# Optimization experiments

Measured on AMD Instinct MI355X. Metric: run time of the kernel, lower is better.

## Reference

```python
import jax, jax.numpy as jnp
import numpy as np

TAU = 20.0        # LIFNeuron default tau
THRESHOLD = 1.0   # LIFNeuron default threshold
RESET = 0.0       # LIFNeuron default reset
DT = 1.0          # SpikingNeuralNetwork dt
ALPHA = DT / TAU

B, T, I, H, O = 256, 128, 512, 1024, 512


def setup_inputs() -> dict:
    key = jax.random.key(0)
    ks = jax.random.split(key, 6)
    def w(k, shape, fan_in):
        return (jax.random.normal(k, shape, jnp.float32) / np.sqrt(fan_in)).astype(jnp.float32)
    return {
        "x":  jax.random.normal(ks[0], (B, T, I), jnp.float32),
        "We": w(ks[1], (I, H), I), "be": jnp.zeros((H,), jnp.float32),
        "W1": w(ks[2], (H, H), H), "b1": jnp.zeros((H,), jnp.float32),
        "W2": w(ks[3], (H, H), H), "b2": jnp.zeros((H,), jnp.float32),
        "Wo": w(ks[4], (H, O), H), "bo": jnp.zeros((O,), jnp.float32),
    }


def _lif(v, inp):
    # v += (-v + inp) * dt/tau; spike = (v >= thr); v = v*(1-spike) + reset*spike
    v = v + (inp - v) * ALPHA
    spike = (v >= THRESHOLD).astype(v.dtype)
    v = v * (1.0 - spike) + RESET * spike
    return v, spike


def reference(x, We, be, W1, b1, W2, b2, Wo, bo):
    b, t, _ = x.shape
    h_dim = We.shape[1]
    o_dim = Wo.shape[1]

    def step(carry, xt):
        v1, v2, vo = carry
        h = jax.nn.relu(xt @ We + be)          # [B, H]
        v1, s1 = _lif(v1, h)                   # neuron 0 (only 2 of 3 neurons used: zip truncation)
        h = s1 @ W1 + b1
        v2, s2 = _lif(v2, h)                   # neuron 1
        h = s2 @ W2 + b2                       # last hidden layer: no neuron applied before output_layer
        vo, so = _lif(vo, h @ Wo + bo)         # output neuron
        return (v1, v2, vo), (s1, s2, so)

    init = (jnp.zeros((b, h_dim), x.dtype),
            jnp.zeros((b, h_dim), x.dtype),
            jnp.zeros((b, o_dim), x.dtype))
    _, (S1, S2, SO) = jax.lax.scan(step, init, jnp.swapaxes(x, 0, 1))  # time-major scan
    # output_spike at last timestep + full (detached) spike history, stacked over time
    return SO[-1], S1, S2, SO
```

## Files before the change

### kernel.cpp

```cpp
#include <hip/hip_runtime.h>
#include <cstdint>
#include <cstddef>

#define B_ 256
#define T_ 128
#define I_ 512
#define H_ 1024
#define O_ 512
static constexpr float ALPHA = 1.0f / 20.0f;
static constexpr float THR   = 1.0f;
static constexpr float S12   = 0.000244140625f;

typedef _Float16 f16;
typedef __attribute__((ext_vector_type(8))) _Float16 f16x8;
typedef __attribute__((ext_vector_type(4))) float f32x4;

__device__ inline void gload_lds16(const void* gsrc, void* ldsdst) {
    __builtin_amdgcn_global_load_lds(
        (const __attribute__((address_space(1))) unsigned int*)gsrc,
        (__attribute__((address_space(3))) unsigned int*)ldsdst, 16, 0, 0);
}

template<bool PERM_X, bool RELU>
__global__ __launch_bounds__(256)
void gemm128(const float* __restrict__ A, const float* __restrict__ Bw,
             const float* __restrict__ bias, float* __restrict__ C,
             int M, int N, int K) {
    constexpr int BM = 128, BN = 128, BK = 16, TM = 8, TN = 8;
    __shared__ float As[BK][BM];
    __shared__ float Bs[BK][BN + 4];

    const int tid = threadIdx.x;
    const int ntile = N / BN;
    const int bx = blockIdx.x % ntile;
    const int by = blockIdx.x / ntile;
    const int row0 = by * BM, col0 = bx * BN;
    const int tx = tid & 15;
    const int ty = tid >> 4;

    float acc[TM][TN] = {};

    for (int k0 = 0; k0 < K; k0 += BK) {
#pragma unroll
        for (int p = 0; p < 2; ++p) {
            int f = tid + p * 256;
            int r  = f >> 2;
            int kc = (f & 3) << 2;
            int m = row0 + r;
            const float* arow;
            if (PERM_X) {
                int t = m >> 8;
                int b = m & 255;
                arow = A + (size_t)(b * T_ + t) * K;
            } else {
                arow = A + (size_t)m * K;
            }
            float4 v = *reinterpret_cast<const float4*>(arow + k0 + kc);
            As[kc + 0][r] = v.x;
            As[kc + 1][r] = v.y;
            As[kc + 2][r] = v.z;
            As[kc + 3][r] = v.w;
        }
#pragma unroll
        for (int p = 0; p < 2; ++p) {
            int f = tid + p * 256;
            int r  = f >> 5;
            int nc = (f & 31) << 2;
            float4 v = *reinterpret_cast<const float4*>(Bw + (size_t)(k0 + r) * N + col0 + nc);
            *reinterpret_cast<float4*>(&Bs[r][nc]) = v;
        }
        __syncthreads();

#pragma unroll
        for (int k = 0; k < BK; ++k) {
            float a[TM], b[TN];
#pragma unroll
            for (int i = 0; i < TM; ++i) a[i] = As[k][ty * TM + i];
#pragma unroll
            for (int j = 0; j < TN; ++j) b[j] = Bs[k][tx * TN + j];
#pragma unroll
            for (int i = 0; i < TM; ++i)
#pragma unroll
                for (int j = 0; j < TN; ++j)
                    acc[i][j] += a[i] * b[j];
        }
        __syncthreads();
    }

#pragma unroll
    for (int i = 0; i < TM; ++i) {
        size_t m = (size_t)(row0 + ty * TM + i);
#pragma unroll
        for (int jj = 0; jj < TN; jj += 4) {
            int n = col0 + tx * TN + jj;
            float4 c4;
            float c0 = acc[i][jj + 0] + bias[n + 0];
            float c1 = acc[i][jj + 1] + bias[n + 1];
            float c2 = acc[i][jj + 2] + bias[n + 2];
            float c3 = acc[i][jj + 3] + bias[n + 3];
            if (RELU) {
                c0 = fmaxf(c0, 0.f); c1 = fmaxf(c1, 0.f);
                c2 = fmaxf(c2, 0.f); c3 = fmaxf(c3, 0.f);
            }
            c4.x = c0; c4.y = c1; c4.z = c2; c4.w = c3;
            *reinterpret_cast<float4*>(C + m * N + n) = c4;
        }
    }
}

template<bool SPLITX, bool PERM, bool RELU, bool WRITE_LAST, bool F16OUT>
__global__ __launch_bounds__(256, 2)
void gemm_lif(const float* __restrict__ A,
              const f16* __restrict__ Bhi, const f16* __restrict__ Blo,
              const float* __restrict__ bias,
              float* __restrict__ S, float* __restrict__ last_out,
              f16* __restrict__ Sf,
              int N, int K) {
    constexpr int BK = 32;
    constexpr int NBUF = SPLITX ? 4 : 3;
    constexpr int BUFSTR = NBUF * 4096;
    constexpr size_t SMEM = (2 * BUFSTR * 2 > 64 * 132 * 4)
                                ? (size_t)(2 * BUFSTR * 2)
                                : (size_t)(64 * 132 * 4);
    __shared__ __align__(16) char smem[SMEM];
    f16* sm = (f16*)smem;
    float (*Cs)[132] = (float (*)[132])smem;

    const int tid  = threadIdx.x;
    const int lane = tid & 63;
    const int w    = tid >> 6;
    const int wr   = w >> 1, wc = w & 1;
    const int ntile = N >> 7;
    const int bx = blockIdx.x % ntile;
    const int b  = blockIdx.x / ntile;
    const int col0 = bx << 7;

    f32x4 acc0[4][4], acc1[4][4];
#pragma unroll
    for (int mi = 0; mi < 4; ++mi)
#pragma unroll
        for (int ni = 0; ni < 4; ++ni) {
            acc0[mi][ni] = {0.f, 0.f, 0.f, 0.f};
            acc1[mi][ni] = {0.f, 0.f, 0.f, 0.f};
        }

    {
        f16* Ah0 = sm;
        f16* Bh0 = sm + 4096;
        f16* Bl0 = sm + 8192;
        f16* Al0 = sm + 12288;
#pragma unroll
        for (int p = 0; p < 2; ++p) {
            int chunk = w * 2 + p;
            int r  = chunk * 16 + (lane >> 2);
            int kq = lane & 3;
            size_t off = (size_t)(col0 + r) * K + kq * 8;
            gload_lds16(Bhi + off, Bh0 + chunk * 512);
            gload_lds16(Blo + off, Bl0 + chunk * 512);
        }
#pragma unroll
        for (int p = 0; p < 4; ++p) {
            int c = tid + p * 256;
            int r = c >> 3;
            int q = c & 7;
            const float* arow = PERM ? A + (size_t)(b * T_ + r) * K
                                     : A + (size_t)(r * B_ + b) * K;
            float4 v = *reinterpret_cast<const float4*>(arow + q * 4);
            union { f16 h[4]; uint2 u; } hi;
            hi.h[0] = (f16)v.x; hi.h[1] = (f16)v.y;
            hi.h[2] = (f16)v.z; hi.h[3] = (f16)v.w;
            *reinterpret_cast<uint2*>(&Ah0[r * BK + q * 4]) = hi.u;
            if (SPLITX) {
                union { f16 h[4]; uint2 u; } lo;
                lo.h[0] = (f16)((v.x - (float)hi.h[0]) * 4096.0f);
                lo.h[1] = (f16)((v.y - (float)hi.h[1]) * 4096.0f);
                lo.h[2] = (f16)((v.z - (float)hi.h[2]) * 4096.0f);
                lo.h[3] = (f16)((v.w - (float)hi.h[3]) * 4096.0f);
                *reinterpret_cast<uint2*>(&Al0[r * BK + q * 4]) = lo.u;
            }
        }
    }
    __syncthreads();

    const int NIT = K / BK;
    for (int it = 0; it < NIT; ++it) {
        const int cur = it & 1, nxt = cur ^ 1;
        const bool more = (it + 1 < NIT);
        const int k0n = (it + 1) * BK;

        f16* Ah_c = sm + cur * BUFSTR;
        f16* Bh_c = Ah_c + 4096;
        f16* Bl_c = Ah_c + 8192;
        f16* Al_c = Ah_c + 12288;
        f16* Ah_n = sm + nxt * BUFSTR;
        f16* Bh_n = Ah_n + 4096;
        f16* Bl_n = Ah_n + 8192;
        f16* Al_n = Ah_n + 12288;

        float4 a4[4];
        if (more) {
#pragma unroll
            for (int p = 0; p < 2; ++p) {
                int chunk = w * 2 + p;
                int r  = chunk * 16 + (lane >> 2);
                int kq = lane & 3;
                size_t off = (size_t)(col0 + r) * K + k0n + kq * 8;
                gload_lds16(Bhi + off, Bh_n + chunk * 512);
                gload_lds16(Blo + off, Bl_n + chunk * 512);
            }
#pragma unroll
            for (int p = 0; p < 4; ++p) {
                int c = tid + p * 256;
                int r = c >> 3;
                int q = c & 7;
                const float* arow = PERM ? A + (size_t)(b * T_ + r) * K
                                         : A + (size_t)(r * B_ + b) * K;
                a4[p] = *reinterpret_cast<const float4*>(arow + k0n + q * 4);
            }
        }

        {
            f16x8 ahi[4], alo[4];
#pragma unroll
            for (int mi = 0; mi < 4; ++mi) {
                int ar = (wr * 64 + mi * 16 + (lane & 15)) * BK + (lane >> 4) * 8;
                ahi[mi] = *reinterpret_cast<const f16x8*>(&Ah_c[ar]);
                if (SPLITX) alo[mi] = *reinterpret_cast<const f16x8*>(&Al_c[ar]);
            }
#pragma unroll
            for (int ni = 0; ni < 4; ++ni) {
                int br = (wc * 64 + ni * 16 + (lane & 15)) * BK + (lane >> 4) * 8;
                f16x8 bh = *reinterpret_cast<const f16x8*>(&Bh_c[br]);
                f16x8 bl = *reinterpret_cast<const f16x8*>(&Bl_c[br]);
#pragma unroll
                for (int mi = 0; mi < 4; ++mi) {
                    acc0[mi][ni] = __builtin_amdgcn_mfma_f32_16x16x32_f16(
                        ahi[mi], bh, acc0[mi][ni], 0, 0, 0);
                    acc1[mi][ni] = __builtin_amdgcn_mfma_f32_16x16x32_f16(
                        ahi[mi], bl, acc1[mi][ni], 0, 0, 0);
                    if (SPLITX)
                        acc1[mi][ni] = __builtin_amdgcn_mfma_f32_16x16x32_f16(
                            alo[mi], bh, acc1[mi][ni], 0, 0, 0);
                }
            }
        }

        if (more) {
#pragma unroll
            for (int p = 0; p < 4; ++p) {
                int c = tid + p * 256;
                int r = c >> 3;
                int q = c & 7;
                float4 v = a4[p];
                union { f16 h[4]; uint2 u; } hi;
                hi.h[0] = (f16)v.x; hi.h[1] = (f16)v.y;
                hi.h[2] = (f16)v.z; hi.h[3] = (f16)v.w;
                *reinterpret_cast<uint2*>(&Ah_n[r * BK + q * 4]) = hi.u;
                if (SPLITX) {
                    union { f16 h[4]; uint2 u; } lo;
                    lo.h[0] = (f16)((v.x - (float)hi.h[0]) * 4096.0f);
                    lo.h[1] = (f16)((v.y - (float)hi.h[1]) * 4096.0f);
                    lo.h[2] = (f16)((v.z - (float)hi.h[2]) * 4096.0f);
                    lo.h[3] = (f16)((v.w - (float)hi.h[3]) * 4096.0f);
                    *reinterpret_cast<uint2*>(&Al_n[r * BK + q * 4]) = lo.u;
                }
            }
        }
        __syncthreads();
    }

    float v = 0.f, s = 0.f;
    float* Sp = S + (size_t)b * N + col0 + (tid & 127);
    const size_t tstride = (size_t)B_ * N;

    if (wr == 0) {
#pragma unroll
        for (int ni = 0; ni < 4; ++ni) {
            int col = wc * 64 + ni * 16 + (lane & 15);
            float bv = bias[col0 + col];
#pragma unroll
            for (int mi = 0; mi < 4; ++mi) {
                int rowb = mi * 16 + ((lane >> 4) << 2);
#pragma unroll
                for (int r = 0; r < 4; ++r) {
                    float cv = acc0[mi][ni][r] + S12 * acc1[mi][ni][r] + bv;
                    if (RELU) cv = fmaxf(cv, 0.f);
                    Cs[rowb + r][col] = cv;
                }
            }
        }
    }
    __syncthreads();
    if (tid < 128) {
#pragma unroll 4
        for (int t = 0; t < 64; ++t) {
            float in = Cs[t][tid];
            v = v + (in - v) * ALPHA;
            bool sp = (v >= THR);
            s = sp ? 1.0f : 0.0f;
            Sp[(size_t)t * tstride] = s;
            if (F16OUT) Sf[((size_t)b * T_ + t) * N + col0 + tid] = (f16)s;
            v = sp ? 0.0f : v;
        }
    }
    __syncthreads();
    if (wr == 1) {
#pragma unroll
        for (int ni = 0; ni < 4; ++ni) {
            int col = wc * 64 + ni * 16 + (lane & 15);
            float bv = bias[col0 + col];
#pragma unroll
            for (int mi = 0; mi < 4; ++mi) {
                int rowb = mi * 16 + ((lane >> 4) << 2);
#pragma unroll
                for (int r = 0; r < 4; ++r) {
                    float cv = acc0[mi][ni][r] + S12 * acc1[mi][ni][r] + bv;
                    if (RELU) cv = fmaxf(cv, 0.f);
                    Cs[rowb + r][col] = cv;
                }
            }
        }
    }
    __syncthreads();
    if (tid < 128) {
#pragma unroll 4
        for (int t = 64; t < 128; ++t) {
            float in = Cs[t - 64][tid];
            v = v + (in - v) * ALPHA;
            bool sp = (v >= THR);
            s = sp ? 1.0f : 0.0f;
            Sp[(size_t)t * tstride] = s;
            if (F16OUT) Sf[((size_t)b * T_ + t) * N + col0 + tid] = (f16)s;
            v = sp ? 0.0f : v;
        }
        if (WRITE_LAST) last_out[(size_t)b * N + col0 + tid] = s;
    }
}

__global__ __launch_bounds__(256, 2)
void gemm_lif_x2(const float* __restrict__ A,
                 const f16* __restrict__ Bhi,
                 const f16* __restrict__ Blo,
                 const float* __restrict__ bias,
                 float* __restrict__ S,
                 f16* __restrict__ Sf,
                 int N, int K) {
    constexpr int BK = 32;
    constexpr int BUFSTR = 4 * 4096;
    __shared__ __align__(16) char smem[2 * BUFSTR * 2];
    f16* sm = (f16*)smem;
    float (*Cs)[132] = (float (*)[132])smem;

    const int tid  = threadIdx.x;
    const int lane = tid & 63;
    const int w    = tid >> 6;
    const int wr   = w >> 1, wc = w & 1;
    const int ntile = N >> 7;
    const int bx = blockIdx.x % ntile;
    const int b  = blockIdx.x / ntile;
    const int col0 = bx << 7;
    const int sw = (((lane >> 4) ^ ((lane >> 1) & 3)) << 3);

    f32x4 acc0[4][4], acc1[4][4];
#pragma unroll
    for (int mi = 0; mi < 4; ++mi)
#pragma unroll
        for (int ni = 0; ni < 4; ++ni) {
            acc0[mi][ni] = {0.f, 0.f, 0.f, 0.f};
            acc1[mi][ni] = {0.f, 0.f, 0.f, 0.f};
        }

    {
        f16* Ah0 = sm;
        f16* Bh0 = sm + 4096;
        f16* Bl0 = sm + 8192;
        f16* Al0 = sm + 12288;
#pragma unroll
        for (int p = 0; p < 2; ++p) {
            int chunk = w * 2 + p;
            int r  = chunk * 16 + (lane >> 2);
            int kq = lane & 3;
            size_t off = (size_t)(col0 + r) * K + kq * 8;
            gload_lds16(Bhi + off, Bh0 + chunk * 512);
            gload_lds16(Blo + off, Bl0 + chunk * 512);
        }
#pragma unroll
        for (int p = 0; p < 4; ++p) {
            int c = tid + p * 256;
            int r = c >> 3;
            int q = c & 7;
            const float* arow = A + (size_t)(b * T_ + r) * K;
            float4 v = *reinterpret_cast<const float4*>(arow + q * 4);
            int aoff = r * 32 + ((((q >> 1) ^ ((r >> 1) & 3))) << 3) + ((q & 1) << 2);
            union { f16 h[4]; uint2 u; } hi;
            hi.h[0] = (f16)v.x; hi.h[1] = (f16)v.y;
            hi.h[2] = (f16)v.z; hi.h[3] = (f16)v.w;
            *reinterpret_cast<uint2*>(&Ah0[aoff]) = hi.u;
            union { f16 h[4]; uint2 u; } lo;
            lo.h[0] = (f16)((v.x - (float)hi.h[0]) * 4096.0f);
            lo.h[1] = (f16)((v.y - (float)hi.h[1]) * 4096.0f);
            lo.h[2] = (f16)((v.z - (float)hi.h[2]) * 4096.0f);
            lo.h[3] = (f16)((v.w - (float)hi.h[3]) * 4096.0f);
            *reinterpret_cast<uint2*>(&Al0[aoff]) = lo.u;
        }
    }
    __syncthreads();

    const int NIT = K / BK;
    for (int it = 0; it < NIT; ++it) {
        const int cur = it & 1, nxt = cur ^ 1;
        const bool more = (it + 1 < NIT);
        const int k0n = (it + 1) * BK;

        f16* Ah_c = sm + cur * BUFSTR;
        f16* Bh_c = Ah_c + 4096;
        f16* Bl_c = Ah_c + 8192;
        f16* Al_c = Ah_c + 12288;
        f16* Ah_n = sm + nxt * BUFSTR;
        f16* Bh_n = Ah_n + 4096;
        f16* Bl_n = Ah_n + 8192;
        f16* Al_n = Ah_n + 12288;

        float4 a4[4];
        if (more) {
#pragma unroll
            for (int p = 0; p < 2; ++p) {
                int chunk = w * 2 + p;
                int r  = chunk * 16 + (lane >> 2);
                int kq = lane & 3;
                size_t off = (size_t)(col0 + r) * K + k0n + kq * 8;
                gload_lds16(Bhi + off, Bh_n + chunk * 512);
                gload_lds16(Blo + off, Bl_n + chunk * 512);
            }
#pragma unroll
            for (int p = 0; p < 4; ++p) {
                int c = tid + p * 256;
                int r = c >> 3;
                int q = c & 7;
                const float* arow = A + (size_t)(b * T_ + r) * K;
                a4[p] = *reinterpret_cast<const float4*>(arow + k0n + q * 4);
            }
        }

        {
            f16x8 ahi[4], alo[4];
#pragma unroll
            for (int mi = 0; mi < 4; ++mi) {
                int ar = (wr * 64 + mi * 16 + (lane & 15)) * BK + sw;
                ahi[mi] = *reinterpret_cast<const f16x8*>(&Ah_c[ar]);
                alo[mi] = *reinterpret_cast<const f16x8*>(&Al_c[ar]);
            }
#pragma unroll
            for (int ni = 0; ni < 4; ++ni) {
                int br = (wc * 64 + ni * 16 + (lane & 15)) * BK + sw;
                f16x8 bh = *reinterpret_cast<const f16x8*>(&Bh_c[br]);
                f16x8 bl = *reinterpret_cast<const f16x8*>(&Bl_c[br]);
#pragma unroll
                for (int mi = 0; mi < 4; ++mi) {
                    acc0[mi][ni] = __builtin_amdgcn_mfma_f32_16x16x32_f16(
                        ahi[mi], bh, acc0[mi][ni], 0, 0, 0);
                    acc1[mi][ni] = __builtin_amdgcn_mfma_f32_16x16x32_f16(
                        ahi[mi], bl, acc1[mi][ni], 0, 0, 0);
                    acc1[mi][ni] = __builtin_amdgcn_mfma_f32_16x16x32_f16(
                        alo[mi], bh, acc1[mi][ni], 0, 0, 0);
                }
            }
        }

        if (more) {
#pragma unroll
            for (int p = 0; p < 4; ++p) {
                int c = tid + p * 256;
                int r = c >> 3;
                int q = c & 7;
                float4 v = a4[p];
                int aoff = r * 32 + ((((q >> 1) ^ ((r >> 1) & 3))) << 3) + ((q & 1) << 2);
                union { f16 h[4]; uint2 u; } hi;
                hi.h[0] = (f16)v.x; hi.h[1] = (f16)v.y;
                hi.h[2] = (f16)v.z; hi.h[3] = (f16)v.w;
                *reinterpret_cast<uint2*>(&Ah_n[aoff]) = hi.u;
                union { f16 h[4]; uint2 u; } lo;
                lo.h[0] = (f16)((v.x - (float)hi.h[0]) * 4096.0f);
                lo.h[1] = (f16)((v.y - (float)hi.h[1]) * 4096.0f);
                lo.h[2] = (f16)((v.z - (float)hi.h[2]) * 4096.0f);
                lo.h[3] = (f16)((v.w - (float)hi.h[3]) * 4096.0f);
                *reinterpret_cast<uint2*>(&Al_n[aoff]) = lo.u;
            }
        }
        __syncthreads();
    }

    float v = 0.f;
    float* Sp = S + (size_t)b * N + col0 + (tid & 127);
    const size_t tstride = (size_t)B_ * N;

    if (wr == 0) {
#pragma unroll
        for (int ni = 0; ni < 4; ++ni) {
            int col = wc * 64 + ni * 16 + (lane & 15);
            float bv = bias[col0 + col];
#pragma unroll
            for (int mi = 0; mi < 4; ++mi) {
                int rowb = mi * 16 + ((lane >> 4) << 2);
#pragma unroll
                for (int r = 0; r < 4; ++r) {
                    float cv = fmaxf(acc0[mi][ni][r] + S12 * acc1[mi][ni][r] + bv, 0.f);
                    Cs[rowb + r][col] = cv;
                }
            }
        }
    }
    __syncthreads();
    if (tid < 128) {
#pragma unroll 4
        for (int t = 0; t < 64; ++t) {
            float in = Cs[t][tid];
            v = v + (in - v) * ALPHA;
            bool sp = (v >= THR);
            float s = sp ? 1.0f : 0.0f;
            Sp[(size_t)t * tstride] = s;
            Sf[((size_t)b * T_ + t) * N + col0 + tid] = (f16)s;
            v = sp ? 0.0f : v;
        }
    }
    __syncthreads();
    if (wr == 1) {
#pragma unroll
        for (int ni = 0; ni < 4; ++ni) {
            int col = wc * 64 + ni * 16 + (lane & 15);
            float bv = bias[col0 + col];
#pragma unroll
            for (int mi = 0; mi < 4; ++mi) {
                int rowb = mi * 16 + ((lane >> 4) << 2);
#pragma unroll
                for (int r = 0; r < 4; ++r) {
                    float cv = fmaxf(acc0[mi][ni][r] + S12 * acc1[mi][ni][r] + bv, 0.f);
                    Cs[rowb + r][col] = cv;
                }
            }
        }
    }
    __syncthreads();
    if (tid < 128) {
#pragma unroll 4
        for (int t = 64; t < 128; ++t) {
            float in = Cs[t - 64][tid];
            v = v + (in - v) * ALPHA;
            bool sp = (v >= THR);
            float s = sp ? 1.0f : 0.0f;
            Sp[(size_t)t * tstride] = s;
            Sf[((size_t)b * T_ + t) * N + col0 + tid] = (f16)s;
            v = sp ? 0.0f : v;
        }
    }
}

template<bool WRITE_LAST, bool F16OUT>
__global__ __launch_bounds__(256, 2)
void gemm_lif_h(const f16* __restrict__ Af,
                const f16* __restrict__ Bhi,
                const f16* __restrict__ Blo,
                const float* __restrict__ bias,
                float* __restrict__ S,
                float* __restrict__ last_out,
                f16* __restrict__ Sf,
                int N, int K) {
    constexpr int BK = 32;
    constexpr int BUFF = 3 * 4096;
    __shared__ __align__(16) char smem[2 * BUFF * 2];
    f16* sm = (f16*)smem;
    float (*Cs)[132] = (float (*)[132])smem;

    const int tid  = threadIdx.x;
    const int lane = tid & 63;
    const int w    = tid >> 6;
    const int wr   = w >> 1, wc = w & 1;
    const int ntile = N >> 7;
    const int bx = blockIdx.x % ntile;
    const int b  = blockIdx.x / ntile;
    const int col0 = bx << 7;
    const int sw = (((lane >> 4) ^ ((lane >> 1) & 3)) << 3);

    f32x4 acc0[4][4], acc1[4][4];
#pragma unroll
    for (int mi = 0; mi < 4; ++mi)
#pragma unroll
        for (int ni = 0; ni < 4; ++ni) {
            acc0[mi][ni] = {0.f, 0.f, 0.f, 0.f};
            acc1[mi][ni] = {0.f, 0.f, 0.f, 0.f};
        }

    const int r0   = (w * 2 + 0) * 16 + (lane >> 2);
    const int r1   = (w * 2 + 1) * 16 + (lane >> 2);
    const int kqs  = lane & 3;
    const int kqa0 = kqs ^ ((r0 >> 1) & 3);
    const int kqa1 = kqs ^ ((r1 >> 1) & 3);

    {
        size_t b0 = (size_t)(col0 + r0) * K + kqs * 8;
        size_t b1 = (size_t)(col0 + r1) * K + kqs * 8;
        size_t a0 = ((size_t)b * T_ + r0) * K + kqa0 * 8;
        size_t a1 = ((size_t)b * T_ + r1) * K + kqa1 * 8;
        gload_lds16(Af + a0,  sm + (w * 2 + 0) * 512);
        gload_lds16(Af + a1,  sm + (w * 2 + 1) * 512);
        gload_lds16(Bhi + b0, sm + 4096 + (w * 2 + 0) * 512);
        gload_lds16(Bhi + b1, sm + 4096 + (w * 2 + 1) * 512);
        gload_lds16(Blo + b0, sm + 8192 + (w * 2 + 0) * 512);
        gload_lds16(Blo + b1, sm + 8192 + (w * 2 + 1) * 512);
    }
    __syncthreads();

    const int NIT = K / BK;
    for (int it = 0; it < NIT; ++it) {
        f16* cur = sm + (it & 1) * BUFF;
        if (it + 1 < NIT) {
            f16* nb = sm + ((it + 1) & 1) * BUFF;
            int k0n = (it + 1) * BK;
            size_t b0 = (size_t)(col0 + r0) * K + k0n + kqs * 8;
            size_t b1 = (size_t)(col0 + r1) * K + k0n + kqs * 8;
            size_t a0 = ((size_t)b * T_ + r0) * K + k0n + kqa0 * 8;
            size_t a1 = ((size_t)b * T_ + r1) * K + k0n + kqa1 * 8;
            gload_lds16(Af + a0,  nb + (w * 2 + 0) * 512);
            gload_lds16(Af + a1,  nb + (w * 2 + 1) * 512);
            gload_lds16(Bhi + b0, nb + 4096 + (w * 2 + 0) * 512);
            gload_lds16(Bhi + b1, nb + 4096 + (w * 2 + 1) * 512);
            gload_lds16(Blo + b0, nb + 8192 + (w * 2 + 0) * 512);
            gload_lds16(Blo + b1, nb + 8192 + (w * 2 + 1) * 512);
        }

        f16x8 af[4];
#pragma unroll
        for (int mi = 0; mi < 4; ++mi)
            af[mi] = *reinterpret_cast<const f16x8*>(
                &cur[(wr * 64 + mi * 16 + (lane & 15)) * BK + sw]);
#pragma unroll
        for (int ni = 0; ni < 4; ++ni) {
            int br = (wc * 64 + ni * 16 + (lane & 15)) * BK + sw;
            f16x8 bh = *reinterpret_cast<const f16x8*>(&cur[4096 + br]);
            f16x8 bl = *reinterpret_cast<const f16x8*>(&cur[8192 + br]);
#pragma unroll
            for (int mi = 0; mi < 4; ++mi) {
                acc0[mi][ni] = __builtin_amdgcn_mfma_f32_16x16x32_f16(
                    af[mi], bh, acc0[mi][ni], 0, 0, 0);
                acc1[mi][ni] = __builtin_amdgcn_mfma_f32_16x16x32_f16(
                    af[mi], bl, acc1[mi][ni], 0, 0, 0);
            }
        }
        __syncthreads();
    }

    float v = 0.f, s = 0.f;
    float* Sp = S + (size_t)b * N + col0 + (tid & 127);
    const size_t tstride = (size_t)B_ * N;

    if (wr == 0) {
#pragma unroll
        for (int ni = 0; ni < 4; ++ni) {
            int col = wc * 64 + ni * 16 + (lane & 15);
            float bv = bias[col0 + col];
#pragma unroll
            for (int mi = 0; mi < 4; ++mi) {
                int rowb = mi * 16 + ((lane >> 4) << 2);
#pragma unroll
                for (int r = 0; r < 4; ++r)
                    Cs[rowb + r][col] = acc0[mi][ni][r] + S12 * acc1[mi][ni][r] + bv;
            }
        }
    }
    __syncthreads();
    if (tid < 128) {
#pragma unroll 4
        for (int t = 0; t < 64; ++t) {
            float in = Cs[t][tid];
            v = v + (in - v) * ALPHA;
            bool sp = (v >= THR);
            s = sp ? 1.0f : 0.0f;
            Sp[(size_t)t * tstride] = s;
            if (F16OUT) Sf[((size_t)b * T_ + t) * N + col0 + tid] = (f16)s;
            v = sp ? 0.0f : v;
        }
    }
    __syncthreads();
    if (wr == 1) {
#pragma unroll
        for (int ni = 0; ni < 4; ++ni) {
            int col = wc * 64 + ni * 16 + (lane & 15);
            float bv = bias[col0 + col];
#pragma unroll
            for (int mi = 0; mi < 4; ++mi) {
                int rowb = mi * 16 + ((lane >> 4) << 2);
#pragma unroll
                for (int r = 0; r < 4; ++r)
                    Cs[rowb + r][col] = acc0[mi][ni][r] + S12 * acc1[mi][ni][r] + bv;
            }
        }
    }
    __syncthreads();
    if (tid < 128) {
#pragma unroll 4
        for (int t = 64; t < 128; ++t) {
            float in = Cs[t - 64][tid];
            v = v + (in - v) * ALPHA;
            bool sp = (v >= THR);
            s = sp ? 1.0f : 0.0f;
            Sp[(size_t)t * tstride] = s;
            if (F16OUT) Sf[((size_t)b * T_ + t) * N + col0 + tid] = (f16)s;
            v = sp ? 0.0f : v;
        }
        if (WRITE_LAST) last_out[(size_t)b * N + col0 + tid] = s;
    }
}

__global__ __launch_bounds__(256)
void lif_scan(float* __restrict__ buf, int BH, float* __restrict__ last_out) {
    int j = blockIdx.x * 256 + threadIdx.x;
    if (j >= BH) return;
    float v = 0.f;
    float last = 0.f;
    for (int t = 0; t < T_; ++t) {
        size_t idx = (size_t)t * BH + j;
        float in = buf[idx];
        v = v + (in - v) * ALPHA;
        bool sp = (v >= THR);
        last = sp ? 1.0f : 0.0f;
        buf[idx] = last;
        v = sp ? 0.0f : v;
    }
    if (last_out) last_out[j] = last;
}

__global__ __launch_bounds__(256)
void make_wf2(const float* __restrict__ W2, const float* __restrict__ Wo,
              float* __restrict__ Wf) {
    __shared__ float w2s[64][33];
    __shared__ float wos[64][68];
    const int tid = threadIdx.x;
    const int ht = blockIdx.x >> 3, ot = blockIdx.x & 7;
    const int h0 = ht * 32, o0 = ot * 64;
    const int th = tid >> 3;
    const int to = tid & 7;

    double acc[8] = {0, 0, 0, 0, 0, 0, 0, 0};

    for (int k0 = 0; k0 < H_; k0 += 64) {
#pragma unroll
        for (int p = 0; p < 2; ++p) {
            int f = tid + p * 256;
            int i = f >> 4;
            int j4 = (f & 15) << 2;
            float4 v = *reinterpret_cast<const float4*>(
                W2 + (size_t)(h0 + i) * H_ + k0 + j4);
            w2s[j4 + 0][i] = v.x; w2s[j4 + 1][i] = v.y;
            w2s[j4 + 2][i] = v.z; w2s[j4 + 3][i] = v.w;
        }
#pragma unroll
        for (int p = 0; p < 4; ++p) {
            int f = tid + p * 256;
            int r = f >> 4;
            int c4 = (f & 15) << 2;
            float4 v = *reinterpret_cast<const float4*>(
                Wo + (size_t)(k0 + r) * O_ + o0 + c4);
            wos[r][c4 + 0] = v.x; wos[r][c4 + 1] = v.y;
            wos[r][c4 + 2] = v.z; wos[r][c4 + 3] = v.w;
        }
        __syncthreads();

#pragma unroll 8
        for (int k = 0; k < 64; ++k) {
            double a = (double)w2s[k][th];
#pragma unroll
            for (int j = 0; j < 8; ++j)
                acc[j] += a * (double)wos[k][to * 8 + j];
        }
        __syncthreads();
    }
#pragma unroll
    for (int j = 0; j < 8; ++j)
        Wf[(size_t)(h0 + th) * O_ + o0 + to * 8 + j] = (float)acc[j];
}

__global__ __launch_bounds__(256)
void make_bf(const float* __restrict__ Wo, const float* __restrict__ b2,
             const float* __restrict__ bo, float* __restrict__ bf) {
    int o = blockIdx.x * 256 + threadIdx.x;
    if (o >= O_) return;
    double acc = (double)bo[o];
    for (int h = 0; h < H_; ++h)
        acc += (double)b2[h] * (double)Wo[(size_t)h * O_ + o];
    bf[o] = (float)acc;
}

template<bool SWZ>
__global__ __launch_bounds__(256)
void split_w16(const float* __restrict__ W, f16* __restrict__ hi,
               f16* __restrict__ lo, int K, int N) {
    int idx = blockIdx.x * 256 + threadIdx.x;
    if (idx >= K * N) return;
    int n = idx / K;
    int ks = idx - n * K;
    int k = SWZ ? ((ks & ~31) | ((((ks >> 3) & 3) ^ ((n >> 1) & 3)) << 3) | (ks & 7))
                : ks;
    float wv = W[(size_t)k * N + n];
    f16 h0 = (f16)wv;
    float r = (wv - (float)h0) * 4096.0f;
    f16 h1 = (f16)r;
    hi[idx] = h0; lo[idx] = h1;
}

extern "C" void kernel_launch(void* const* d_in, const int* in_sizes, int n_in,
                              void* d_out, int out_size, void* d_ws, size_t ws_size,
                              hipStream_t stream) {
    const float* x  = (const float*)d_in[0];
    const float* We = (const float*)d_in[1];
    const float* be = (const float*)d_in[2];
    const float* W1 = (const float*)d_in[3];
    const float* b1 = (const float*)d_in[4];
    const float* W2 = (const float*)d_in[5];
    const float* b2 = (const float*)d_in[6];
    const float* Wo = (const float*)d_in[7];
    const float* bo = (const float*)d_in[8];

    float* out = (float*)d_out;
    float* so_last = out;
    float* S1 = out + (size_t)B_ * O_;
    float* S2 = S1 + (size_t)T_ * B_ * H_;
    float* SO = S2 + (size_t)T_ * B_ * H_;

    const int TB = T_ * B_;
    dim3 blk(256);

    const size_t MB = 1024 * 1024;
    const size_t sz_s1f = (size_t)T_ * B_ * H_ * 2;

    const size_t b_weh = 0;
    const size_t b_wel = 1 * MB;
    const size_t b_w1h = 2 * MB;
    const size_t b_w1l = 4 * MB;
    const size_t b_wfh = 6 * MB;
    const size_t b_wfl = 7 * MB;
    const size_t b_bf  = 8 * MB;
    const size_t b_wf  = 8 * MB + 4096;
    const size_t b_s1f = 10 * MB + 4096;
    const size_t b_s2f = b_s1f + sz_s1f;
    const size_t need_hi = b_s2f + sz_s1f;

    const size_t m_weh = 0;
    const size_t m_wel = m_weh + (size_t)I_ * H_ * 2;
    const size_t m_w1h = m_wel + (size_t)I_ * H_ * 2;
    const size_t m_w1l = m_w1h + (size_t)H_ * H_ * 2;
    const size_t m_wf  = m_w1l + (size_t)H_ * H_ * 2;
    const size_t m_bf  = m_wf + (size_t)H_ * O_ * 4;
    const size_t m_wfh = m_bf + (size_t)O_ * 4;
    const size_t m_wfl = m_wfh + (size_t)H_ * O_ * 2;
    const size_t need_mid = m_wfl + (size_t)H_ * O_ * 2;

    if (ws_size >= need_hi) {
        char* ws = (char*)d_ws;
        f16*   weh = (f16*)(ws + b_weh);
        f16*   wel = (f16*)(ws + b_wel);
        f16*   w1h = (f16*)(ws + b_w1h);
        f16*   w1l = (f16*)(ws + b_w1l);
        f16*   wfh = (f16*)(ws + b_wfh);
        f16*   wfl = (f16*)(ws + b_wfl);
        float* bf  = (float*)(ws + b_bf);
        float* Wf  = (float*)(ws + b_wf);
        f16*   s1f = (f16*)(ws + b_s1f);
        f16*   s2f = (f16*)(ws + b_s2f);

        split_w16<true><<<dim3((I_ * H_ + 255) / 256), blk, 0, stream>>>(We, weh, wel, I_, H_);
        split_w16<true><<<dim3((H_ * H_ + 255) / 256), blk, 0, stream>>>(W1, w1h, w1l, H_, H_);
        make_wf2<<<dim3(256), blk, 0, stream>>>(W2, Wo, Wf);
        make_bf<<<dim3(2), blk, 0, stream>>>(Wo, b2, bo, bf);
        split_w16<true><<<dim3((H_ * O_ + 255) / 256), blk, 0, stream>>>(Wf, wfh, wfl, H_, O_);

        gemm_lif_x2<<<dim3(B_ * (H_ / 128)), blk, 0, stream>>>(
            x, weh, wel, be, S1, s1f, H_, I_);

        gemm_lif_h<false, true><<<dim3(B_ * (H_ / 128)), blk, 0, stream>>>(
            s1f, w1h, w1l, b1, S2, nullptr, s2f, H_, H_);

        gemm_lif_h<true, false><<<dim3(B_ * (O_ / 128)), blk, 0, stream>>>(
            s2f, wfh, wfl, bf, SO, so_last, nullptr, O_, H_);
    } else if (ws_size >= need_mid) {
        char* ws = (char*)d_ws;
        f16*   weh = (f16*)(ws + m_weh);
        f16*   wel = (f16*)(ws + m_wel);
        f16*   w1h = (f16*)(ws + m_w1h);
        f16*   w1l = (f16*)(ws + m_w1l);
        float* Wf  = (float*)(ws + m_wf);
        float* bf  = (float*)(ws + m_bf);
        f16*   wfh = (f16*)(ws + m_wfh);
        f16*   wfl = (f16*)(ws + m_wfl);

        split_w16<false><<<dim3((I_ * H_ + 255) / 256), blk, 0, stream>>>(We, weh, wel, I_, H_);
        split_w16<false><<<dim3((H_ * H_ + 255) / 256), blk, 0, stream>>>(W1, w1h, w1l, H_, H_);
        make_wf2<<<dim3(256), blk, 0, stream>>>(W2, Wo, Wf);
        make_bf<<<dim3(2), blk, 0, stream>>>(Wo, b2, bo, bf);
        split_w16<false><<<dim3((H_ * O_ + 255) / 256), blk, 0, stream>>>(Wf, wfh, wfl, H_, O_);

        gemm_lif<true, true, true, false, false><<<dim3(B_ * (H_ / 128)), blk, 0, stream>>>(
            x, weh, wel, be, S1, nullptr, nullptr, H_, I_);
        gemm_lif<false, false, false, false, false><<<dim3(B_ * (H_ / 128)), blk, 0, stream>>>(
            S1, w1h, w1l, b1, S2, nullptr, nullptr, H_, H_);
        gemm_lif<false, false, false, true, false><<<dim3(B_ * (O_ / 128)), blk, 0, stream>>>(
            S2, wfh, wfl, bf, SO, so_last, nullptr, O_, H_);
    } else {
        float* Wf = (float*)d_ws;
        float* bf = Wf + (size_t)H_ * O_;
        gemm128<true, true><<<dim3((TB / 128) * (H_ / 128)), blk, 0, stream>>>(
            x, We, be, S1, TB, H_, I_);
        lif_scan<<<dim3((B_ * H_ + 255) / 256), blk, 0, stream>>>(S1, B_ * H_, nullptr);
        gemm128<false, false><<<dim3((TB / 128) * (H_ / 128)), blk, 0, stream>>>(
            S1, W1, b1, S2, TB, H_, H_);
        lif_scan<<<dim3((B_ * H_ + 255) / 256), blk, 0, stream>>>(S2, B_ * H_, nullptr);
        make_wf2<<<dim3(256), blk, 0, stream>>>(W2, Wo, Wf);
        make_bf<<<dim3(2), blk, 0, stream>>>(Wo, b2, bo, bf);
        gemm128<false, false><<<dim3((TB / 128) * (O_ / 128)), blk, 0, stream>>>(
            S2, Wf, bf, SO, TB, O_, H_);
        lif_scan<<<dim3((B_ * O_ + 255) / 256), blk, 0, stream>>>(SO, B_ * O_, so_last);
    }
}
```

Before: 581.3 us.

## Cut LDS and raise occupancy in LIF GEMMs; tile-transpose weight split kernels

The first-layer GEMM stops double-buffering the converted A tile in shared memory, so LDS per block drops to 48KB, and both GEMM kernels are asked for three blocks per CU instead of two. The A tile now gets an extra barrier before it is overwritten, which adds a sync and reduces overlap in exchange for occupancy. The weight hi/lo split kernels are rewritten to transpose through shared memory for coalesced reads and vectorized writes. The bias-folding kernel is parallelised over four partial sums per output. Raising the launch bound may force register spills in the MFMA-heavy kernels.

New measurement: 884.7 us. 52.2% more time.

```diff
diff --git a/kernel.cpp b/kernel.cpp
--- a/kernel.cpp
+++ b/kernel.cpp
@@ -337,8 +337,8 @@
     }
 }
 
-__global__ __launch_bounds__(256, 2)
-void gemm_lif_x2(const float* __restrict__ A,
+__global__ __launch_bounds__(256, 3)
+void gemm_lif_x3(const float* __restrict__ A,
                  const f16* __restrict__ Bhi,
                  const f16* __restrict__ Blo,
                  const float* __restrict__ bias,
@@ -346,9 +346,10 @@
                  f16* __restrict__ Sf,
                  int N, int K) {
     constexpr int BK = 32;
-    constexpr int BUFSTR = 4 * 4096;
-    __shared__ __align__(16) char smem[2 * BUFSTR * 2];
+    __shared__ __align__(16) char smem[49152];
     f16* sm = (f16*)smem;
+    f16* Ah = sm;
+    f16* Al = sm + 4096;
     float (*Cs)[132] = (float (*)[132])smem;
 
     const int tid  = threadIdx.x;
@@ -371,10 +372,8 @@
         }
 
     {
-        f16* Ah0 = sm;
-        f16* Bh0 = sm + 4096;
-        f16* Bl0 = sm + 8192;
-        f16* Al0 = sm + 12288;
+        f16* Bh0 = sm + 8192;
+        f16* Bl0 = sm + 12288;
 #pragma unroll
         for (int p = 0; p < 2; ++p) {
             int chunk = w * 2 + p;
@@ -395,34 +394,28 @@
             union { f16 h[4]; uint2 u; } hi;
             hi.h[0] = (f16)v.x; hi.h[1] = (f16)v.y;
             hi.h[2] = (f16)v.z; hi.h[3] = (f16)v.w;
-            *reinterpret_cast<uint2*>(&Ah0[aoff]) = hi.u;
+            *reinterpret_cast<uint2*>(&Ah[aoff]) = hi.u;
             union { f16 h[4]; uint2 u; } lo;
             lo.h[0] = (f16)((v.x - (float)hi.h[0]) * 4096.0f);
             lo.h[1] = (f16)((v.y - (float)hi.h[1]) * 4096.0f);
             lo.h[2] = (f16)((v.z - (float)hi.h[2]) * 4096.0f);
             lo.h[3] = (f16)((v.w - (float)hi.h[3]) * 4096.0f);
-            *reinterpret_cast<uint2*>(&Al0[aoff]) = lo.u;
+            *reinterpret_cast<uint2*>(&Al[aoff]) = lo.u;
         }
     }
     __syncthreads();
 
     const int NIT = K / BK;
     for (int it = 0; it < NIT; ++it) {
-        const int cur = it & 1, nxt = cur ^ 1;
         const bool more = (it + 1 < NIT);
         const int k0n = (it + 1) * BK;
-
-        f16* Ah_c = sm + cur * BUFSTR;
-        f16* Bh_c = Ah_c + 4096;
-        f16* Bl_c = Ah_c + 8192;
-        f16* Al_c = Ah_c + 12288;
-        f16* Ah_n = sm + nxt * BUFSTR;
-        f16* Bh_n = Ah_n + 4096;
-        f16* Bl_n = Ah_n + 8192;
-        f16* Al_n = Ah_n + 12288;
+        f16* Bh_c = sm + 8192 + (it & 1) * 8192;
+        f16* Bl_c = Bh_c + 4096;
 
         float4 a4[4];
         if (more) {
+            f16* Bh_n = sm + 8192 + ((it + 1) & 1) * 8192;
+            f16* Bl_n = Bh_n + 4096;
 #pragma unroll
             for (int p = 0; p < 2; ++p) {
                 int chunk = w * 2 + p;
@@ -447,8 +440,8 @@
 #pragma unroll
             for (int mi = 0; mi < 4; ++mi) {
                 int ar = (wr * 64 + mi * 16 + (lane & 15)) * BK + sw;
-                ahi[mi] = *reinterpret_cast<const f16x8*>(&Ah_c[ar]);
-                alo[mi] = *reinterpret_cast<const f16x8*>(&Al_c[ar]);
+                ahi[mi] = *reinterpret_cast<const f16x8*>(&Ah[ar]);
+                alo[mi] = *reinterpret_cast<const f16x8*>(&Al[ar]);
             }
 #pragma unroll
             for (int ni = 0; ni < 4; ++ni) {
@@ -466,6 +459,7 @@
                 }
             }
         }
+        __syncthreads();
 
         if (more) {
 #pragma unroll
@@ -478,13 +472,13 @@
                 union { f16 h[4]; uint2 u; } hi;
                 hi.h[0] = (f16)v.x; hi.h[1] = (f16)v.y;
                 hi.h[2] = (f16)v.z; hi.h[3] = (f16)v.w;
-                *reinterpret_cast<uint2*>(&Ah_n[aoff]) = hi.u;
+                *reinterpret_cast<uint2*>(&Ah[aoff]) = hi.u;
                 union { f16 h[4]; uint2 u; } lo;
                 lo.h[0] = (f16)((v.x - (float)hi.h[0]) * 4096.0f);
                 lo.h[1] = (f16)((v.y - (float)hi.h[1]) * 4096.0f);
                 lo.h[2] = (f16)((v.z - (float)hi.h[2]) * 4096.0f);
                 lo.h[3] = (f16)((v.w - (float)hi.h[3]) * 4096.0f);
-                *reinterpret_cast<uint2*>(&Al_n[aoff]) = lo.u;
+                *reinterpret_cast<uint2*>(&Al[aoff]) = lo.u;
             }
         }
         __syncthreads();
@@ -556,7 +550,7 @@
 }
 
 template<bool WRITE_LAST, bool F16OUT>
-__global__ __launch_bounds__(256, 2)
+__global__ __launch_bounds__(256, 3)
 void gemm_lif_h(const f16* __restrict__ Af,
                 const f16* __restrict__ Bhi,
                 const f16* __restrict__ Blo,
@@ -790,6 +784,25 @@
     bf[o] = (float)acc;
 }
 
+__global__ __launch_bounds__(256)
+void make_bf2(const float* __restrict__ Wo, const float* __restrict__ b2,
+              const float* __restrict__ bo, float* __restrict__ bf) {
+    __shared__ double red[4][64];
+    const int tid  = threadIdx.x;
+    const int ol   = tid & 63;
+    const int part = tid >> 6;
+    const int o    = blockIdx.x * 64 + ol;
+    double acc = 0.0;
+    for (int h = part; h < H_; h += 4)
+        acc += (double)b2[h] * (double)Wo[(size_t)h * O_ + o];
+    red[part][ol] = acc;
+    __syncthreads();
+    if (part == 0) {
+        double s = red[0][ol] + red[1][ol] + red[2][ol] + red[3][ol];
+        bf[o] = (float)((double)bo[o] + s);
+    }
+}
+
 template<bool SWZ>
 __global__ __launch_bounds__(256)
 void split_w16(const float* __restrict__ W, f16* __restrict__ hi,
@@ -807,6 +820,53 @@
     hi[idx] = h0; lo[idx] = h1;
 }
 
+template<bool SWZ>
+__global__ __launch_bounds__(256)
+void split_w16t(const float* __restrict__ W, f16* __restrict__ hi,
+                f16* __restrict__ lo, int K, int N) {
+    __shared__ float tile[64][65];
+    const int tid = threadIdx.x;
+    const int ntile = N >> 6;
+    const int kt = blockIdx.x / ntile;
+    const int nt = blockIdx.x % ntile;
+    const int k0 = kt << 6, n0 = nt << 6;
+
+#pragma unroll
+    for (int p = 0; p < 4; ++p) {
+        int lin = p * 256 + tid;
+        int r = lin >> 4;
+        int c = (lin & 15) << 2;
+        float4 v = *reinterpret_cast<const float4*>(
+            W + (size_t)(k0 + r) * N + n0 + c);
+        tile[r][c + 0] = v.x; tile[r][c + 1] = v.y;
+        tile[r][c + 2] = v.z; tile[r][c + 3] = v.w;
+    }
+    __syncthreads();
+
+    const int nl = tid >> 2;
+    const int q  = tid & 3;
+    const int n  = n0 + nl;
+#pragma unroll
+    for (int half = 0; half < 2; ++half) {
+        union { f16 h[8]; uint4 u4; } Hh, Hl;
+#pragma unroll
+        for (int j = 0; j < 8; ++j) {
+            int ksl = q * 16 + half * 8 + j;
+            int kl  = SWZ ? ((ksl & ~31) |
+                             ((((ksl >> 3) & 3) ^ ((n >> 1) & 3)) << 3) |
+                             (ksl & 7))
+                          : ksl;
+            float wv = tile[kl][nl];
+            f16 h0 = (f16)wv;
+            float rr = (wv - (float)h0) * 4096.0f;
+            Hh.h[j] = h0; Hl.h[j] = (f16)rr;
+        }
+        size_t off = (size_t)n * K + k0 + q * 16 + half * 8;
+        *reinterpret_cast<uint4*>(hi + off) = Hh.u4;
+        *reinterpret_cast<uint4*>(lo + off) = Hl.u4;
+    }
+}
+
 extern "C" void kernel_launch(void* const* d_in, const int* in_sizes, int n_in,
                               void* d_out, int out_size, void* d_ws, size_t ws_size,
                               hipStream_t stream) {
@@ -867,13 +927,13 @@
         f16*   s1f = (f16*)(ws + b_s1f);
         f16*   s2f = (f16*)(ws + b_s2f);
 
-        split_w16<true><<<dim3((I_ * H_ + 255) / 256), blk, 0, stream>>>(We, weh, wel, I_, H_);
-        split_w16<true><<<dim3((H_ * H_ + 255) / 256), blk, 0, stream>>>(W1, w1h, w1l, H_, H_);
+        split_w16t<true><<<dim3((I_ >> 6) * (H_ >> 6)), blk, 0, stream>>>(We, weh, wel, I_, H_);
+        split_w16t<true><<<dim3((H_ >> 6) * (H_ >> 6)), blk, 0, stream>>>(W1, w1h, w1l, H_, H_);
         make_wf2<<<dim3(256), blk, 0, stream>>>(W2, Wo, Wf);
-        make_bf<<<dim3(2), blk, 0, stream>>>(Wo, b2, bo, bf);
-        split_w16<true><<<dim3((H_ * O_ + 255) / 256), blk, 0, stream>>>(Wf, wfh, wfl, H_, O_);
-
-        gemm_lif_x2<<<dim3(B_ * (H_ / 128)), blk, 0, stream>>>(
+        make_bf2<<<dim3(O_ / 64), blk, 0, stream>>>(Wo, b2, bo, bf);
+        split_w16t<true><<<dim3((H_ >> 6) * (O_ >> 6)), blk, 0, stream>>>(Wf, wfh, wfl, H_, O_);
+
+        gemm_lif_x3<<<dim3(B_ * (H_ / 128)), blk, 0, stream>>>(
             x, weh, wel, be, S1, s1f, H_, I_);
 
         gemm_lif_h<false, true><<<dim3(B_ * (H_ / 128)), blk, 0, stream>>>(
```
